# Performance work log

Hardware: AMD Instinct MI355X
Metric: run time of the kernel (lower is better)

Reference implementation:

```python
import jax, jax.numpy as jnp
import numpy as np

BN_EPS = 1e-5


def setup_inputs() -> dict:
    key = jax.random.key(0)
    k0, k1, k2 = jax.random.split(key, 3)
    N, K, Cin, Cout = 300000, 27, 32, 64
    data = jax.random.normal(k0, (N, Cin), dtype=jnp.float32)
    # Octree neighbor table: index of the neighbor node for each of the 27
    # stencil offsets (-1 would mean empty; here all indices are valid).
    neigh = jax.random.randint(k1, (N, K), 0, N, dtype=jnp.int64)
    # Conv weight, one [Cin, Cout] matrix per stencil offset.
    weight = jax.random.normal(k2, (K, Cin, Cout), dtype=jnp.float32) * (1.0 / np.sqrt(K * Cin))
    gamma = jnp.ones((Cout,), dtype=jnp.float32)
    beta = jnp.zeros((Cout,), dtype=jnp.float32)
    return {"data": data, "neigh": neigh, "weight": weight, "gamma": gamma, "beta": beta}


def reference(data, neigh, weight, gamma, beta):
    # --- OctreeConv: gather neighbors (im2col over sparse octree) + matmul ---
    mask = neigh >= 0                                   # [N, K] valid-neighbor mask
    idx = jnp.clip(neigh, 0)
    gathered = jnp.where(mask[..., None], data[idx], 0.0)  # [N, K, Cin]
    out = jnp.einsum('nkc,kco->no', gathered, weight)       # [N, Cout]
    # --- BatchNorm1d (training mode: batch statistics over nodes) ---
    mean = jnp.mean(out, axis=0)
    var = jnp.var(out, axis=0)
    out = (out - mean) * jax.lax.rsqrt(var + BN_EPS) * gamma + beta
    # --- ReLU ---
    return jax.nn.relu(out)
```

## Files before the change

kernel.cpp:

```cpp
#include <hip/hip_runtime.h>

#define N_NODES   300000
#define K_STENCIL 27
#define CIN       32
#define COUT      64
#define BN_EPS    1e-5f

#define WS_STATS_OFF 0
#define WS_AB_OFF    32768
#define WS_WT_OFF    33280
#define N_SPLITS     64

typedef short bf16x8 __attribute__((ext_vector_type(8)));
typedef float f32x4  __attribute__((ext_vector_type(4)));

__device__ __forceinline__ short f2bf_rne(float f) {
    unsigned u = __builtin_bit_cast(unsigned, f);
    u += 0x7fffu + ((u >> 16) & 1u);
    return (short)(u >> 16);
}

__global__ void prep(const float* __restrict__ w, unsigned short* __restrict__ wT,
                     float* __restrict__ stats) {
    int t = blockIdx.x * blockDim.x + threadIdx.x;
    if (t < N_SPLITS * 128) stats[t] = 0.f;
    if (t < K_STENCIL * COUT * CIN) {
        int c = t & (CIN - 1);
        int o = (t >> 5) & (COUT - 1);
        int k = t >> 11;
        wT[t] = (unsigned short)f2bf_rne(w[(k * CIN + c) * COUT + o]);
    }
}

__global__ __launch_bounds__(256, 2) void conv_mfma(
        const float* __restrict__ data, const int* __restrict__ neigh,
        const unsigned short* __restrict__ wT, float* __restrict__ out) {
    const int wave  = threadIdx.x >> 6;
    const int lane  = threadIdx.x & 63;
    const int row16 = lane & 15;
    const int quad  = lane >> 4;

    bf16x8 ia, tb;
    #pragma unroll
    for (int j = 0; j < 8; ++j) {
        int k = quad * 8 + j;
        ia[j] = (k == row16) ? (short)0x3F80 : (short)0;
        tb[j] = f2bf_rne((float)(k * 16 + row16));
    }
    f32x4 pacc = {0.f, 0.f, 0.f, 0.f};
    pacc = __builtin_amdgcn_mfma_f32_16x16x32_bf16(ia, tb, pacc, 0, 0, 0);
    int mrow[4], ncol[4];
    #pragma unroll
    for (int r = 0; r < 4; ++r) {
        int iv = (int)(pacc[r] + 0.5f);
        mrow[r] = (iv >> 4) & 15;
        ncol[r] = iv & 15;
    }

    const int node   = blockIdx.x * 64 + wave * 16 + row16;
    const bool valid = (node < N_NODES);
    const int nclamp = valid ? node : 0;

    f32x4 acc[4] = {f32x4{0,0,0,0}, f32x4{0,0,0,0}, f32x4{0,0,0,0}, f32x4{0,0,0,0}};
    const int* nrow = neigh + nclamp * K_STENCIL;

    #pragma unroll
    for (int g = 0; g < 3; ++g) {
        int kid[9];
        #pragma unroll
        for (int j = 0; j < 9; ++j) kid[j] = nrow[g * 9 + j];

        f32x4 lo[9], hi[9];
        #pragma unroll
        for (int j = 0; j < 9; ++j) {
            int idx = kid[j];
            if (valid && idx >= 0) {
                const f32x4* drow = (const f32x4*)(data + (size_t)idx * CIN + quad * 8);
                lo[j] = drow[0];
                hi[j] = drow[1];
            } else {
                lo[j] = f32x4{0, 0, 0, 0};
                hi[j] = f32x4{0, 0, 0, 0};
            }
        }

        #pragma unroll
        for (int j = 0; j < 9; ++j) {
            bf16x8 afrag;
            #pragma unroll
            for (int t = 0; t < 4; ++t) {
                afrag[t]     = f2bf_rne(lo[j][t]);
                afrag[t + 4] = f2bf_rne(hi[j][t]);
            }
            const unsigned short* wk = wT + (g * 9 + j) * (COUT * CIN) + row16 * CIN + quad * 8;
            #pragma unroll
            for (int ct = 0; ct < 4; ++ct) {
                bf16x8 bfrag = *(const bf16x8*)(wk + ct * 16 * CIN);
                acc[ct] = __builtin_amdgcn_mfma_f32_16x16x32_bf16(afrag, bfrag, acc[ct], 0, 0, 0);
            }
        }
    }

    const int tilebase = blockIdx.x * 64 + wave * 16;
    #pragma unroll
    for (int ct = 0; ct < 4; ++ct) {
        #pragma unroll
        for (int r = 0; r < 4; ++r) {
            int n_out = tilebase + mrow[r];
            if (n_out < N_NODES)
                out[(size_t)n_out * COUT + ct * 16 + ncol[r]] = acc[ct][r];
        }
    }
}

__global__ __launch_bounds__(256) void stats_pass(const float* __restrict__ out,
                                                  float* __restrict__ stats) {
    __shared__ float lsum[COUT];
    __shared__ float lsq[COUT];
    if (threadIdx.x < COUT) { lsum[threadIdx.x] = 0.f; lsq[threadIdx.x] = 0.f; }
    __syncthreads();

    const int j = threadIdx.x & 15;
    int row = blockIdx.x * 16 + (threadIdx.x >> 4);
    const int rstride = gridDim.x * 16;
    float s0=0,s1=0,s2=0,s3=0,q0=0,q1=0,q2=0,q3=0;
    for (; row < N_NODES; row += rstride) {
        f32x4 v = ((const f32x4*)out)[row * 16 + j];
        s0 += v[0]; q0 += v[0]*v[0];
        s1 += v[1]; q1 += v[1]*v[1];
        s2 += v[2]; q2 += v[2]*v[2];
        s3 += v[3]; q3 += v[3]*v[3];
    }
    atomicAdd(&lsum[j*4+0], s0); atomicAdd(&lsq[j*4+0], q0);
    atomicAdd(&lsum[j*4+1], s1); atomicAdd(&lsq[j*4+1], q1);
    atomicAdd(&lsum[j*4+2], s2); atomicAdd(&lsq[j*4+2], q2);
    atomicAdd(&lsum[j*4+3], s3); atomicAdd(&lsq[j*4+3], q3);
    __syncthreads();

    if (threadIdx.x < 128) {
        int split = blockIdx.x & (N_SPLITS - 1);
        float v = (threadIdx.x < 64) ? lsum[threadIdx.x] : lsq[threadIdx.x - 64];
        atomicAdd(&stats[split * 128 + threadIdx.x], v);
    }
}

__global__ void finalize_stats(const float* __restrict__ stats,
                               const float* __restrict__ gamma,
                               const float* __restrict__ beta,
                               float* __restrict__ ab) {
    int o = threadIdx.x;
    if (o >= COUT) return;
    float s = 0.f, q = 0.f;
    for (int sp = 0; sp < N_SPLITS; ++sp) {
        s += stats[sp * 128 + o];
        q += stats[sp * 128 + 64 + o];
    }
    float inv_n = 1.0f / (float)N_NODES;
    float mean = s * inv_n;
    float var  = q * inv_n - mean * mean;
    float a = gamma[o] * rsqrtf(var + BN_EPS);
    float b = beta[o] - mean * a;
    ab[o] = a;
    ab[64 + o] = b;
}

__global__ __launch_bounds__(256) void bn_relu(float* __restrict__ out,
                                               const float* __restrict__ ab) {
    int i = blockIdx.x * blockDim.x + threadIdx.x;
    f32x4 a = ((const f32x4*)ab)[i & 15];
    f32x4 b = ((const f32x4*)(ab + 64))[i & 15];
    f32x4 v = ((f32x4*)out)[i];
    #pragma unroll
    for (int j = 0; j < 4; ++j) {
        float y = v[j] * a[j] + b[j];
        v[j] = y > 0.f ? y : 0.f;
    }
    ((f32x4*)out)[i] = v;
}

extern "C" void kernel_launch(void* const* d_in, const int* in_sizes, int n_in,
                              void* d_out, int out_size, void* d_ws, size_t ws_size,
                              hipStream_t stream) {
    const float* data   = (const float*)d_in[0];
    const int*   neigh  = (const int*)d_in[1];
    const float* weight = (const float*)d_in[2];
    const float* gamma  = (const float*)d_in[3];
    const float* beta   = (const float*)d_in[4];
    float* out = (float*)d_out;

    char* ws = (char*)d_ws;
    float*          stats = (float*)(ws + WS_STATS_OFF);
    float*          ab    = (float*)(ws + WS_AB_OFF);
    unsigned short* wT    = (unsigned short*)(ws + WS_WT_OFF);

    prep<<<(K_STENCIL * COUT * CIN + 255) / 256, 256, 0, stream>>>(weight, wT, stats);

    const int grid = (N_NODES + 63) / 64;
    conv_mfma<<<grid, 256, 0, stream>>>(data, neigh, wT, out);

    stats_pass<<<1024, 256, 0, stream>>>(out, stats);
    finalize_stats<<<1, 64, 0, stream>>>(stats, gamma, beta, ab);

    int total4 = N_NODES * COUT / 4;
    bn_relu<<<total4 / 256, 256, 0, stream>>>(out, ab);
}
```

Baseline: 397.5 us.

## Pre-convert data to bf16 and fuse BN statistics into conv kernel

Adds a prep step that converts the input features to bf16 in workspace when space allows, so the conv kernel gathers half as many bytes per neighbor and issues all 27 gathers before the MFMA loop. BN sum and sum-of-squares are now accumulated in the conv epilogue through shared-memory atomics, which removes the separate stats pass that re-read the whole output. The costs are an extra full pass over the data for conversion, more registers to hold 27 gathered fragments, and LDS atomic contention in the epilogue.

After: 560.9 us. 1.41x slower.

```diff
diff --git a/kernel.cpp b/kernel.cpp
--- a/kernel.cpp
+++ b/kernel.cpp
@@ -9,6 +9,7 @@
 #define WS_STATS_OFF 0
 #define WS_AB_OFF    32768
 #define WS_WT_OFF    33280
+#define WS_DATA_OFF  143872
 #define N_SPLITS     64
 
 typedef short bf16x8 __attribute__((ext_vector_type(8)));
@@ -20,8 +21,12 @@
     return (short)(u >> 16);
 }
 
-__global__ void prep(const float* __restrict__ w, unsigned short* __restrict__ wT,
-                     float* __restrict__ stats) {
+__global__ __launch_bounds__(256) void prep(const float* __restrict__ w,
+                                            unsigned short* __restrict__ wT,
+                                            float* __restrict__ stats,
+                                            const float* __restrict__ data,
+                                            unsigned short* __restrict__ dataB,
+                                            int doData) {
     int t = blockIdx.x * blockDim.x + threadIdx.x;
     if (t < N_SPLITS * 128) stats[t] = 0.f;
     if (t < K_STENCIL * COUT * CIN) {
@@ -30,15 +35,117 @@
         int k = t >> 11;
         wT[t] = (unsigned short)f2bf_rne(w[(k * CIN + c) * COUT + o]);
     }
-}
-
-__global__ __launch_bounds__(256, 2) void conv_mfma(
-        const float* __restrict__ data, const int* __restrict__ neigh,
-        const unsigned short* __restrict__ wT, float* __restrict__ out) {
+    if (doData && t < N_NODES * CIN / 8) {
+        const f32x4* src = (const f32x4*)data + (size_t)t * 2;
+        f32x4 a = src[0], b = src[1];
+        bf16x8 o8;
+        #pragma unroll
+        for (int j = 0; j < 4; ++j) {
+            o8[j]     = f2bf_rne(a[j]);
+            o8[j + 4] = f2bf_rne(b[j]);
+        }
+        ((bf16x8*)dataB)[t] = o8;
+    }
+}
+
+__global__ __launch_bounds__(256, 2) void conv_bf16(
+        const unsigned short* __restrict__ dataB, const int* __restrict__ neigh,
+        const unsigned short* __restrict__ wT, float* __restrict__ out,
+        float* __restrict__ stats) {
     const int wave  = threadIdx.x >> 6;
     const int lane  = threadIdx.x & 63;
     const int row16 = lane & 15;
     const int quad  = lane >> 4;
+
+    __shared__ float lsum[COUT];
+    __shared__ float lsq[COUT];
+    if (threadIdx.x < COUT) { lsum[threadIdx.x] = 0.f; lsq[threadIdx.x] = 0.f; }
+
+    bf16x8 ia, tb;
+    #pragma unroll
+    for (int j = 0; j < 8; ++j) {
+        int k = quad * 8 + j;
+        ia[j] = (k == row16) ? (short)0x3F80 : (short)0;
+        tb[j] = f2bf_rne((float)(k * 16 + row16));
+    }
+    f32x4 pacc = {0.f, 0.f, 0.f, 0.f};
+    pacc = __builtin_amdgcn_mfma_f32_16x16x32_bf16(ia, tb, pacc, 0, 0, 0);
+    int mrow[4], ncol[4];
+    #pragma unroll
+    for (int r = 0; r < 4; ++r) {
+        int iv = (int)(pacc[r] + 0.5f);
+        mrow[r] = (iv >> 4) & 15;
+        ncol[r] = iv & 15;
+    }
+
+    const int node   = blockIdx.x * 64 + wave * 16 + row16;
+    const bool valid = (node < N_NODES);
+    const int nclamp = valid ? node : 0;
+    const int* nrow  = neigh + (size_t)nclamp * K_STENCIL;
+
+    int kid[K_STENCIL];
+    #pragma unroll
+    for (int j = 0; j < K_STENCIL; ++j) kid[j] = nrow[j];
+
+    const bf16x8 zfrag = {0, 0, 0, 0, 0, 0, 0, 0};
+    bf16x8 pay[K_STENCIL];
+    #pragma unroll
+    for (int j = 0; j < K_STENCIL; ++j) {
+        int idx = kid[j];
+        if (valid && idx >= 0)
+            pay[j] = *(const bf16x8*)(dataB + (size_t)idx * CIN + quad * 8);
+        else
+            pay[j] = zfrag;
+    }
+    __builtin_amdgcn_sched_barrier(0);
+
+    f32x4 acc[4] = {f32x4{0,0,0,0}, f32x4{0,0,0,0}, f32x4{0,0,0,0}, f32x4{0,0,0,0}};
+    const unsigned short* wbase = wT + row16 * CIN + quad * 8;
+    #pragma unroll
+    for (int j = 0; j < K_STENCIL; ++j) {
+        const unsigned short* wk = wbase + j * (COUT * CIN);
+        #pragma unroll
+        for (int ct = 0; ct < 4; ++ct) {
+            bf16x8 bfrag = *(const bf16x8*)(wk + ct * 16 * CIN);
+            acc[ct] = __builtin_amdgcn_mfma_f32_16x16x32_bf16(pay[j], bfrag, acc[ct], 0, 0, 0);
+        }
+    }
+
+    __syncthreads();
+    const int tilebase = blockIdx.x * 64 + wave * 16;
+    #pragma unroll
+    for (int ct = 0; ct < 4; ++ct) {
+        #pragma unroll
+        for (int r = 0; r < 4; ++r) {
+            int n_out = tilebase + mrow[r];
+            int col   = ct * 16 + ncol[r];
+            float v   = acc[ct][r];
+            if (n_out < N_NODES)
+                out[(size_t)n_out * COUT + col] = v;
+            atomicAdd(&lsum[col], v);
+            atomicAdd(&lsq[col], v * v);
+        }
+    }
+    __syncthreads();
+    if (threadIdx.x < 128) {
+        int split = blockIdx.x & (N_SPLITS - 1);
+        float v = (threadIdx.x < 64) ? lsum[threadIdx.x] : lsq[threadIdx.x - 64];
+        atomicAdd(&stats[split * 128 + threadIdx.x], v);
+    }
+}
+
+__global__ __launch_bounds__(256, 2) void conv_f32(
+        const float* __restrict__ data, const int* __restrict__ neigh,
+        const unsigned short* __restrict__ wT, float* __restrict__ out,
+        float* __restrict__ stats) {
+    const int wave  = threadIdx.x >> 6;
+    const int lane  = threadIdx.x & 63;
+    const int row16 = lane & 15;
+    const int quad  = lane >> 4;
+
+    __shared__ float lsum[COUT];
+    __shared__ float lsq[COUT];
+    if (threadIdx.x < COUT) { lsum[threadIdx.x] = 0.f; lsq[threadIdx.x] = 0.f; }
 
     bf16x8 ia, tb;
     #pragma unroll
@@ -101,42 +208,22 @@
         }
     }
 
+    __syncthreads();
     const int tilebase = blockIdx.x * 64 + wave * 16;
     #pragma unroll
     for (int ct = 0; ct < 4; ++ct) {
         #pragma unroll
         for (int r = 0; r < 4; ++r) {
             int n_out = tilebase + mrow[r];
+            int col   = ct * 16 + ncol[r];
+            float v   = acc[ct][r];
             if (n_out < N_NODES)
-                out[(size_t)n_out * COUT + ct * 16 + ncol[r]] = acc[ct][r];
-        }
-    }
-}
-
-__global__ __launch_bounds__(256) void stats_pass(const float* __restrict__ out,
-                                                  float* __restrict__ stats) {
-    __shared__ float lsum[COUT];
-    __shared__ float lsq[COUT];
-    if (threadIdx.x < COUT) { lsum[threadIdx.x] = 0.f; lsq[threadIdx.x] = 0.f; }
+                out[(size_t)n_out * COUT + col] = v;
+            atomicAdd(&lsum[col], v);
+            atomicAdd(&lsq[col], v * v);
+        }
+    }
     __syncthreads();
-
-    const int j = threadIdx.x & 15;
-    int row = blockIdx.x * 16 + (threadIdx.x >> 4);
-    const int rstride = gridDim.x * 16;
-    float s0=0,s1=0,s2=0,s3=0,q0=0,q1=0,q2=0,q3=0;
-    for (; row < N_NODES; row += rstride) {
-        f32x4 v = ((const f32x4*)out)[row * 16 + j];
-        s0 += v[0]; q0 += v[0]*v[0];
-        s1 += v[1]; q1 += v[1]*v[1];
-        s2 += v[2]; q2 += v[2]*v[2];
-        s3 += v[3]; q3 += v[3]*v[3];
-    }
-    atomicAdd(&lsum[j*4+0], s0); atomicAdd(&lsq[j*4+0], q0);
-    atomicAdd(&lsum[j*4+1], s1); atomicAdd(&lsq[j*4+1], q1);
-    atomicAdd(&lsum[j*4+2], s2); atomicAdd(&lsq[j*4+2], q2);
-    atomicAdd(&lsum[j*4+3], s3); atomicAdd(&lsq[j*4+3], q3);
-    __syncthreads();
-
     if (threadIdx.x < 128) {
         int split = blockIdx.x & (N_SPLITS - 1);
         float v = (threadIdx.x < 64) ? lsum[threadIdx.x] : lsq[threadIdx.x - 64];
@@ -192,13 +279,21 @@
     float*          stats = (float*)(ws + WS_STATS_OFF);
     float*          ab    = (float*)(ws + WS_AB_OFF);
     unsigned short* wT    = (unsigned short*)(ws + WS_WT_OFF);
-
-    prep<<<(K_STENCIL * COUT * CIN + 255) / 256, 256, 0, stream>>>(weight, wT, stats);
+    unsigned short* dataB = (unsigned short*)(ws + WS_DATA_OFF);
+
+    const size_t need_bf16 = (size_t)WS_DATA_OFF + (size_t)N_NODES * CIN * 2;
+    const int useBf16 = (ws_size >= need_bf16) ? 1 : 0;
+
+    const int prepGrid = useBf16 ? (N_NODES * CIN / 8 + 255) / 256
+                                 : (K_STENCIL * COUT * CIN + 255) / 256;
+    prep<<<prepGrid, 256, 0, stream>>>(weight, wT, stats, data, dataB, useBf16);
 
     const int grid = (N_NODES + 63) / 64;
-    conv_mfma<<<grid, 256, 0, stream>>>(data, neigh, wT, out);
-
-    stats_pass<<<1024, 256, 0, stream>>>(out, stats);
+    if (useBf16)
+        conv_bf16<<<grid, 256, 0, stream>>>(dataB, neigh, wT, out, stats);
+    else
+        conv_f32<<<grid, 256, 0, stream>>>(data, neigh, wT, out, stats);
+
     finalize_stats<<<1, 64, 0, stream>>>(stats, gamma, beta, ab);
 
     int total4 = N_NODES * COUT / 4;
```
